# Optimization experiments

Measured on AMD Instinct MI355X. Metric: run time of the kernel, lower is better.

Reference implementation:

```python
import math
import jax, jax.numpy as jnp
import numpy as np

NUM_HEADS = 8


def setup_inputs() -> dict:
    rng = jax.random.key(0)
    ks = jax.random.split(rng, 6)
    S, B, E = 2048, 4, 512
    scale = 1.0 / math.sqrt(E)  # xavier-ish init scale
    return {
        "query": jax.random.normal(ks[0], (S, B, E), jnp.float32),
        "key": jax.random.normal(ks[1], (S, B, E), jnp.float32),
        "value": jax.random.normal(ks[2], (S, B, E), jnp.float32),
        "attn_mask": jax.random.normal(ks[3], (B, S, S), jnp.float32),
        "in_proj_weight": jax.random.normal(ks[4], (3 * E, E), jnp.float32) * scale,
        "in_proj_bias": jnp.zeros((3 * E,), jnp.float32),
        "out_proj_weight": jax.random.normal(ks[5], (E, E), jnp.float32) * scale,
        "out_proj_bias": jnp.zeros((E,), jnp.float32),
    }


def reference(query, key, value, attn_mask, in_proj_weight, in_proj_bias,
              out_proj_weight, out_proj_bias):
    # Layout: [S, B, E] (batch_first=False)
    S, B, E = query.shape
    H = NUM_HEADS
    D = E // H
    w_q, w_k, w_v = jnp.split(in_proj_weight, 3, axis=0)  # each [E, E]
    b_q, b_k, b_v = jnp.split(in_proj_bias, 3)
    q = query @ w_q.T + b_q
    k = key @ w_k.T + b_k
    v = value @ w_v.T + b_v

    def to_heads(x):  # [S,B,E] -> [B,H,S,D]
        return x.reshape(S, B, H, D).transpose(1, 2, 0, 3)

    qh = to_heads(q) * (1.0 / math.sqrt(D))
    kh = to_heads(k)
    vh = to_heads(v)
    # full score matrix [B,H,S,S] with per-batch additive mask broadcast over heads
    scores = jnp.einsum('bhsd,bhtd->bhst', qh, kh) + attn_mask[:, None, :, :]
    attn = jax.nn.softmax(scores, axis=-1)
    out = jnp.einsum('bhst,bhtd->bhsd', attn, vh)
    out = out.transpose(2, 0, 1, 3).reshape(S, B, E)  # back to [S,B,E]
    return out @ out_proj_weight.T + out_proj_bias
```

## Files before the change

kernel.cpp:

```cpp
#include <hip/hip_runtime.h>


#define L2E 1.44269504088896340736f

typedef __attribute__((ext_vector_type(8))) __bf16 bf16x8;
typedef __attribute__((ext_vector_type(4))) float f32x4;
typedef __attribute__((ext_vector_type(16))) float f32x16;

static __device__ __forceinline__ unsigned pk2(float a, float b) {
    union { unsigned u; __bf16 h[2]; } cv;
    cv.h[0] = (__bf16)a; cv.h[1] = (__bf16)b;
    return cv.u;
}

static __device__ __forceinline__ unsigned short f2bf(float f) {
    union { unsigned short s; __bf16 h; } cv;
    cv.h = (__bf16)f;
    return cv.s;
}

static __device__ __forceinline__ float bflo(unsigned u) {
    union { unsigned u; float f; } cv; cv.u = u << 16; return cv.f;
}
static __device__ __forceinline__ float bfhi(unsigned u) {
    union { unsigned u; float f; } cv; cv.u = u & 0xFFFF0000u; return cv.f;
}

__global__ __launch_bounds__(256) void qkv_kernel(
    const float* __restrict__ Xq, const float* __restrict__ Xk,
    const float* __restrict__ Xv, const float* __restrict__ W,
    const float* __restrict__ bias,
    unsigned short* __restrict__ Qp, unsigned short* __restrict__ Kp,
    unsigned short* __restrict__ Vt)
{
    __shared__ unsigned short lA[128][40];
    __shared__ unsigned short lB[128][40];

    const int z = blockIdx.z;
    const float* X  = (z == 0) ? Xq : (z == 1) ? Xk : Xv;
    const float* Wz = W + (size_t)z * 512 * 512;
    const int rb = blockIdx.y * 128;
    const int nb = blockIdx.x * 128;
    const int tid  = threadIdx.x;
    const int lane = tid & 63, wave = tid >> 6;
    const int wr = wave >> 1, wc = wave & 1;
    const int lq = lane & 15, lg = lane >> 4;

    f32x4 acc[4][4];
#pragma unroll
    for (int i = 0; i < 4; ++i)
#pragma unroll
        for (int j = 0; j < 4; ++j) acc[i][j] = (f32x4){0.f, 0.f, 0.f, 0.f};

    const int srow = tid >> 1;
    const int scol = (tid & 1) * 16;

    for (int kt = 0; kt < 16; ++kt) {
        const int k0 = kt * 32;
        if (kt) __syncthreads();
        {
            const float* g = X + (size_t)(rb + srow) * 512 + k0 + scol;
            float4 x0 = *(const float4*)(g + 0);
            float4 x1 = *(const float4*)(g + 4);
            float4 x2 = *(const float4*)(g + 8);
            float4 x3 = *(const float4*)(g + 12);
            uint4 w0, w1;
            w0.x = pk2(x0.x, x0.y); w0.y = pk2(x0.z, x0.w);
            w0.z = pk2(x1.x, x1.y); w0.w = pk2(x1.z, x1.w);
            w1.x = pk2(x2.x, x2.y); w1.y = pk2(x2.z, x2.w);
            w1.z = pk2(x3.x, x3.y); w1.w = pk2(x3.z, x3.w);
            *(uint4*)&lA[srow][scol] = w0;
            *(uint4*)&lA[srow][scol + 8] = w1;
        }
        {
            const float* g = Wz + (size_t)(nb + srow) * 512 + k0 + scol;
            float4 x0 = *(const float4*)(g + 0);
            float4 x1 = *(const float4*)(g + 4);
            float4 x2 = *(const float4*)(g + 8);
            float4 x3 = *(const float4*)(g + 12);
            uint4 w0, w1;
            w0.x = pk2(x0.x, x0.y); w0.y = pk2(x0.z, x0.w);
            w0.z = pk2(x1.x, x1.y); w0.w = pk2(x1.z, x1.w);
            w1.x = pk2(x2.x, x2.y); w1.y = pk2(x2.z, x2.w);
            w1.z = pk2(x3.x, x3.y); w1.w = pk2(x3.z, x3.w);
            *(uint4*)&lB[srow][scol] = w0;
            *(uint4*)&lB[srow][scol + 8] = w1;
        }
        __syncthreads();

        bf16x8 af[4], bf[4];
#pragma unroll
        for (int mi = 0; mi < 4; ++mi)
            af[mi] = *(const bf16x8*)&lA[wr * 64 + mi * 16 + lq][lg * 8];
#pragma unroll
        for (int ni = 0; ni < 4; ++ni)
            bf[ni] = *(const bf16x8*)&lB[wc * 64 + ni * 16 + lq][lg * 8];
#pragma unroll
        for (int mi = 0; mi < 4; ++mi)
#pragma unroll
            for (int ni = 0; ni < 4; ++ni)
                acc[mi][ni] = __builtin_amdgcn_mfma_f32_16x16x32_bf16(
                    af[mi], bf[ni], acc[mi][ni], 0, 0, 0);
    }

    const float* bz = bias + z * 512;
#pragma unroll
    for (int ni = 0; ni < 4; ++ni) {
        const int n = nb + wc * 64 + ni * 16 + lq;
        const float bv = bz[n];
        const int h = n >> 6, d = n & 63;
#pragma unroll
        for (int mi = 0; mi < 4; ++mi) {
#pragma unroll
            for (int r = 0; r < 4; ++r) {
                const int t = rb + wr * 64 + mi * 16 + lg * 4 + r;
                float v = acc[mi][ni][r] + bv;
                const int s = t >> 2, b = t & 3;
                if (z == 0) {
                    v *= 0.125f * L2E;
                    Qp[((size_t)(b * 8 + h) * 2048 + s) * 64 + d] = f2bf(v);
                } else if (z == 1) {
                    Kp[((size_t)(b * 8 + h) * 2048 + s) * 64 + d] = f2bf(v);
                } else {
                    Vt[((size_t)(b * 8 + h) * 64 + d) * 2048 + s] = f2bf(v);
                }
            }
        }
    }
}

__global__ __launch_bounds__(256) void maskprep_kernel(
    const float* __restrict__ mask, unsigned short* __restrict__ Mf)
{
    __shared__ float lT[32][261];
    const int tid = threadIdx.x;
    const int bq = blockIdx.y;
    const int kx = blockIdx.x;
    const float* base = mask + ((size_t)(bq >> 6) * 2048 + (bq & 63) * 32) * 2048
                        + (size_t)kx * 256;

    const int r = tid >> 3, ci = tid & 7;
    const float* rp = base + (size_t)r * 2048;
#pragma unroll
    for (int j = 0; j < 8; ++j) {
        const int c = (ci + j * 8) * 4;
        float4 v = *(const float4*)(rp + c);
        lT[r][c + 0] = v.x * L2E;
        lT[r][c + 1] = v.y * L2E;
        lT[r][c + 2] = v.z * L2E;
        lT[r][c + 3] = v.w * L2E;
    }
    __syncthreads();

    const int w = tid >> 6, lane = tid & 63;
    const int lc = lane & 31, hi = lane >> 5;
#pragma unroll
    for (int t = 0; t < 2; ++t) {
        const int ktl = w * 2 + t;
        float p[16];
#pragma unroll
        for (int jj = 0; jj < 16; ++jj)
            p[jj] = lT[lc][ktl * 32 + (jj & 3) + 8 * (jj >> 2) + 4 * hi];
        unsigned short* dst = Mf + ((size_t)bq * 64 + kx * 8 + ktl) * 1024 + lane * 16;
        *(uint4*)(dst) = make_uint4(pk2(p[0], p[1]), pk2(p[2], p[3]),
                                    pk2(p[4], p[5]), pk2(p[6], p[7]));
        *(uint4*)(dst + 8) = make_uint4(pk2(p[8], p[9]),  pk2(p[10], p[11]),
                                        pk2(p[12], p[13]), pk2(p[14], p[15]));
    }
}

#define SWAP32(a, b) asm("v_permlane32_swap_b32 %0, %1" : "+v"(a), "+v"(b))

#define COMPUTE(KC, VC, M) do {                                                \
    bf16x8 pf[4];                                                              \
    _Pragma("unroll")                                                          \
    for (int kblk = 0; kblk < 2; ++kblk) {                                     \
        f32x16 z;                                                              \
        {                                                                      \
            const uint4 m0 = M[kblk][0], m1 = M[kblk][1];                      \
            z[0]  = bflo(m0.x); z[1]  = bfhi(m0.x);                            \
            z[2]  = bflo(m0.y); z[3]  = bfhi(m0.y);                            \
            z[4]  = bflo(m0.z); z[5]  = bfhi(m0.z);                            \
            z[6]  = bflo(m0.w); z[7]  = bfhi(m0.w);                            \
            z[8]  = bflo(m1.x); z[9]  = bfhi(m1.x);                            \
            z[10] = bflo(m1.y); z[11] = bfhi(m1.y);                            \
            z[12] = bflo(m1.z); z[13] = bfhi(m1.z);                            \
            z[14] = bflo(m1.w); z[15] = bfhi(m1.w);                            \
        }                                                                      \
        __builtin_amdgcn_s_setprio(1);                                         \
        _Pragma("unroll")                                                      \
        for (int s = 0; s < 4; ++s) {                                          \
            bf16x8 kf = *(const bf16x8*)((KC) + fof[kblk][s]);                 \
            z = __builtin_amdgcn_mfma_f32_32x32x16_bf16(kf, qf[s], z, 0,0,0);  \
        }                                                                      \
        __builtin_amdgcn_s_setprio(0);                                         \
        float p[16];                                                           \
        _Pragma("unroll")                                                      \
        for (int i = 0; i < 16; ++i) p[i] = exp2f(z[i]);                       \
        lsum += (((p[0]+p[1])+(p[2]+p[3])) + ((p[4]+p[5])+(p[6]+p[7])))        \
              + (((p[8]+p[9])+(p[10]+p[11])) + ((p[12]+p[13])+(p[14]+p[15]))); \
        unsigned a0 = pk2(p[0], p[1]),   b0 = pk2(p[4], p[5]);                 \
        unsigned a1 = pk2(p[2], p[3]),   b1 = pk2(p[6], p[7]);                 \
        SWAP32(a0, b0); SWAP32(a1, b1);                                        \
        union { unsigned w[4]; bf16x8 v; } u0;                                 \
        u0.w[0] = a0; u0.w[1] = a1; u0.w[2] = b0; u0.w[3] = b1;                \
        pf[kblk*2] = u0.v;                                                     \
        unsigned c0 = pk2(p[8], p[9]),   d0 = pk2(p[12], p[13]);               \
        unsigned c1 = pk2(p[10], p[11]), d1 = pk2(p[14], p[15]);               \
        SWAP32(c0, d0); SWAP32(c1, d1);                                        \
        union { unsigned w[4]; bf16x8 v; } u1;                                 \
        u1.w[0] = c0; u1.w[1] = c1; u1.w[2] = d0; u1.w[3] = d1;                \
        pf[kblk*2+1] = u1.v;                                                   \
    }                                                                          \
    __builtin_amdgcn_s_setprio(1);                                             \
    _Pragma("unroll")                                                          \
    for (int s = 0; s < 4; ++s) {                                              \
        bf16x8 vf0 = *(const bf16x8*)((VC) + fof[0][s]);                       \
        o0 = __builtin_amdgcn_mfma_f32_32x32x16_bf16(vf0, pf[s], o0, 0,0,0);   \
        bf16x8 vf1 = *(const bf16x8*)((VC) + fof[1][s]);                       \
        o1 = __builtin_amdgcn_mfma_f32_32x32x16_bf16(vf1, pf[s], o1, 0,0,0);   \
    }                                                                          \
    __builtin_amdgcn_s_setprio(0);                                             \
} while (0)

#define LOADNEXT(MD) do {                                                      \
    ka = *(const uint4*)(pgK); kc = *(const uint4*)(pgK + 8);                  \
    va = *(const uint4*)(pgV); vc = *(const uint4*)(pgV + 8);                  \
    MD[0][0] = *(const uint4*)(pmf);                                           \
    MD[0][1] = *(const uint4*)(pmf + 8);                                       \
    MD[1][0] = *(const uint4*)(pmf + 1024);                                    \
    MD[1][1] = *(const uint4*)(pmf + 1032);                                    \
    pgK += 4096; pgV += 64; pmf += 2048;                                       \
} while (0)

#define STORE(BUF) do {                                                        \
    *(uint4*)&lK[BUF][srow][su0 * 8] = ka;                                     \
    *(uint4*)&lK[BUF][srow][su1 * 8] = kc;                                     \
    *(uint4*)&lV[BUF][srow][su0 * 8] = va;                                     \
    *(uint4*)&lV[BUF][srow][su1 * 8] = vc;                                     \
} while (0)

__global__ __launch_bounds__(256, 2) void attn_kernel(
    const unsigned short* __restrict__ Qp, const unsigned short* __restrict__ Kp,
    const unsigned short* __restrict__ Vt, const unsigned short* __restrict__ Mf,
    unsigned short* __restrict__ AO)
{
    __shared__ unsigned short lK[2][64][64];
    __shared__ unsigned short lV[2][64][64];

    const int bh = blockIdx.y;
    const int b = bh >> 3, h = bh & 7;
    const int qb = blockIdx.x * 128;
    const int tid  = threadIdx.x;
    const int lane = tid & 63, wave = tid >> 6;
    const int lc = lane & 31, hi = lane >> 5;
    const int qg = qb + wave * 32 + lc;

    bf16x8 qf[4];
    {
        const unsigned short* qp = Qp + ((size_t)bh * 2048 + qg) * 64 + hi * 8;
#pragma unroll
        for (int s = 0; s < 4; ++s)
            qf[s] = *(const bf16x8*)(qp + s * 16);
    }

    f32x16 o0, o1;
#pragma unroll
    for (int i = 0; i < 16; ++i) { o0[i] = 0.f; o1[i] = 0.f; }
    float lsum = 0.f;

    int fof[2][4];
#pragma unroll
    for (int blk = 0; blk < 2; ++blk)
#pragma unroll
        for (int s = 0; s < 4; ++s)
            fof[blk][s] = (blk * 32 + lc) * 128 +
                          ((((s << 1) | hi) ^ (lane & 7)) * 16);

    const char* lK0c = (const char*)&lK[0][0][0];
    const char* lK1c = (const char*)&lK[1][0][0];
    const char* lV0c = (const char*)&lV[0][0][0];
    const char* lV1c = (const char*)&lV[1][0][0];

    const int srow = tid >> 2;
    const int scu  = (tid & 3) * 2;
    const int su0  = (scu    ) ^ (srow & 7);
    const int su1  = (scu + 1) ^ (srow & 7);
    const unsigned short* pgK = Kp + (size_t)bh * 2048 * 64 + (size_t)srow * 64 + scu * 8;
    const unsigned short* pgV = Vt + (size_t)bh * 64 * 2048 + (size_t)srow * 2048 + scu * 8;
    const unsigned short* pmf = Mf +
        ((size_t)(b * 64 + (qb >> 5) + wave) * 64) * 1024 + lane * 16;

    uint4 ka, kc, va, vc;
    uint4 mA[2][2], mB[2][2];

    LOADNEXT(mA);
    STORE(0);
    __syncthreads();

    for (int kb2 = 0; kb2 < 16; ++kb2) {
        {
            LOADNEXT(mB);
            COMPUTE(lK0c, lV0c, mA);
            STORE(1);
            __syncthreads();
        }
        {
            if (kb2 < 15) LOADNEXT(mA);
            COMPUTE(lK1c, lV1c, mB);
            if (kb2 < 15) {
                STORE(0);
                __syncthreads();
            }
        }
    }

    lsum += __shfl_xor(lsum, 32);
    const float inv = 1.0f / lsum;

    unsigned short* ao = AO + ((size_t)qg * 4 + b) * 512 + h * 64;
#pragma unroll
    for (int g = 0; g < 4; ++g) {
        const int d0 = g * 8 + hi * 4;
        *(uint2*)(ao + d0) =
            make_uint2(pk2(o0[4*g+0] * inv, o0[4*g+1] * inv),
                       pk2(o0[4*g+2] * inv, o0[4*g+3] * inv));
        *(uint2*)(ao + 32 + d0) =
            make_uint2(pk2(o1[4*g+0] * inv, o1[4*g+1] * inv),
                       pk2(o1[4*g+2] * inv, o1[4*g+3] * inv));
    }
}

__global__ __launch_bounds__(256) void oproj_kernel(
    const unsigned short* __restrict__ A, const float* __restrict__ W,
    const float* __restrict__ bias, float* __restrict__ out)
{
    __shared__ unsigned short lA[128][40];
    __shared__ unsigned short lB[128][40];

    const int rb = blockIdx.y * 128;
    const int nb = blockIdx.x * 128;
    const int tid  = threadIdx.x;
    const int lane = tid & 63, wave = tid >> 6;
    const int wr = wave >> 1, wc = wave & 1;
    const int lq = lane & 15, lg = lane >> 4;

    f32x4 acc[4][4];
#pragma unroll
    for (int i = 0; i < 4; ++i)
#pragma unroll
        for (int j = 0; j < 4; ++j) acc[i][j] = (f32x4){0.f, 0.f, 0.f, 0.f};

    const int srow = tid >> 1;
    const int scol = (tid & 1) * 16;

    for (int kt = 0; kt < 16; ++kt) {
        const int k0 = kt * 32;
        if (kt) __syncthreads();
        {
            const unsigned short* g = A + (size_t)(rb + srow) * 512 + k0 + scol;
            *(uint4*)&lA[srow][scol]     = *(const uint4*)g;
            *(uint4*)&lA[srow][scol + 8] = *(const uint4*)(g + 8);
        }
        {
            const float* g = W + (size_t)(nb + srow) * 512 + k0 + scol;
            float4 x0 = *(const float4*)(g + 0);
            float4 x1 = *(const float4*)(g + 4);
            float4 x2 = *(const float4*)(g + 8);
            float4 x3 = *(const float4*)(g + 12);
            uint4 w0, w1;
            w0.x = pk2(x0.x, x0.y); w0.y = pk2(x0.z, x0.w);
            w0.z = pk2(x1.x, x1.y); w0.w = pk2(x1.z, x1.w);
            w1.x = pk2(x2.x, x2.y); w1.y = pk2(x2.z, x2.w);
            w1.z = pk2(x3.x, x3.y); w1.w = pk2(x3.z, x3.w);
            *(uint4*)&lB[srow][scol] = w0;
            *(uint4*)&lB[srow][scol + 8] = w1;
        }
        __syncthreads();

        bf16x8 af[4], bfr[4];
#pragma unroll
        for (int mi = 0; mi < 4; ++mi)
            af[mi] = *(const bf16x8*)&lA[wr * 64 + mi * 16 + lq][lg * 8];
#pragma unroll
        for (int ni = 0; ni < 4; ++ni)
            bfr[ni] = *(const bf16x8*)&lB[wc * 64 + ni * 16 + lq][lg * 8];
#pragma unroll
        for (int mi = 0; mi < 4; ++mi)
#pragma unroll
            for (int ni = 0; ni < 4; ++ni)
                acc[mi][ni] = __builtin_amdgcn_mfma_f32_16x16x32_bf16(
                    af[mi], bfr[ni], acc[mi][ni], 0, 0, 0);
    }

#pragma unroll
    for (int ni = 0; ni < 4; ++ni) {
        const int n = nb + wc * 64 + ni * 16 + lq;
        const float bv = bias[n];
#pragma unroll
        for (int mi = 0; mi < 4; ++mi) {
#pragma unroll
            for (int r = 0; r < 4; ++r) {
                const int t = rb + wr * 64 + mi * 16 + lg * 4 + r;
                out[(size_t)t * 512 + n] = acc[mi][ni][r] + bv;
            }
        }
    }
}

extern "C" void kernel_launch(void* const* d_in, const int* in_sizes, int n_in,
                              void* d_out, int out_size, void* d_ws, size_t ws_size,
                              hipStream_t stream)
{
    (void)in_sizes; (void)n_in; (void)out_size; (void)ws_size;
    const float* query = (const float*)d_in[0];
    const float* key   = (const float*)d_in[1];
    const float* value = (const float*)d_in[2];
    const float* mask  = (const float*)d_in[3];
    const float* w_in  = (const float*)d_in[4];
    const float* b_in  = (const float*)d_in[5];
    const float* w_out = (const float*)d_in[6];
    const float* b_out = (const float*)d_in[7];
    float* out = (float*)d_out;

    char* ws = (char*)d_ws;
    unsigned short* Qp = (unsigned short*)(ws);
    unsigned short* Kp = (unsigned short*)(ws + (size_t)8 * 1024 * 1024);
    unsigned short* Vt = (unsigned short*)(ws + (size_t)16 * 1024 * 1024);
    unsigned short* AO = (unsigned short*)(ws + (size_t)24 * 1024 * 1024);
    unsigned short* Mf = (unsigned short*)(ws + (size_t)32 * 1024 * 1024);

    qkv_kernel<<<dim3(4, 64, 3), 256, 0, stream>>>(query, key, value, w_in, b_in,
                                                   Qp, Kp, Vt);
    maskprep_kernel<<<dim3(8, 256), 256, 0, stream>>>(mask, Mf);
    attn_kernel<<<dim3(16, 32), 256, 0, stream>>>(Qp, Kp, Vt, Mf, AO);
    oproj_kernel<<<dim3(4, 64), 256, 0, stream>>>(AO, w_out, b_out, out);
}
```

Measured before the change: 154.2 us.

## Split attention key range across two wave groups with LDS reduction

Doubles the attention block to 512 threads. Two wave groups each process half of the key sequence for the same 128 queries, using separate double-buffered K/V LDS tiles. Partial outputs and row sums are then combined through shared memory before normalisation and store. This gives 512 blocks of 8 waves instead of 4, raising parallelism and latency hiding. The cost is 64KB of LDS per block, an extra reduction and barrier, and reliance on the softmax having no running max, so partials can simply be added.

```diff
diff --git a/kernel.cpp b/kernel.cpp
--- a/kernel.cpp
+++ b/kernel.cpp
@@ -234,27 +234,30 @@
 } while (0)
 
 #define STORE(BUF) do {                                                        \
-    *(uint4*)&lK[BUF][srow][su0 * 8] = ka;                                     \
-    *(uint4*)&lK[BUF][srow][su1 * 8] = kc;                                     \
-    *(uint4*)&lV[BUF][srow][su0 * 8] = va;                                     \
-    *(uint4*)&lV[BUF][srow][su1 * 8] = vc;                                     \
+    *(uint4*)&lK[kg][BUF][srow][su0 * 8] = ka;                                 \
+    *(uint4*)&lK[kg][BUF][srow][su1 * 8] = kc;                                 \
+    *(uint4*)&lV[kg][BUF][srow][su0 * 8] = va;                                 \
+    *(uint4*)&lV[kg][BUF][srow][su1 * 8] = vc;                                 \
 } while (0)
 
-__global__ __launch_bounds__(256, 2) void attn_kernel(
+__global__ __launch_bounds__(512, 4) void attn_kernel(
     const unsigned short* __restrict__ Qp, const unsigned short* __restrict__ Kp,
     const unsigned short* __restrict__ Vt, const unsigned short* __restrict__ Mf,
     unsigned short* __restrict__ AO)
 {
-    __shared__ unsigned short lK[2][64][64];
-    __shared__ unsigned short lV[2][64][64];
+    __shared__ __align__(16) char smem[65536];
+    unsigned short (*lK)[2][64][64] = (unsigned short (*)[2][64][64])(smem);
+    unsigned short (*lV)[2][64][64] = (unsigned short (*)[2][64][64])(smem + 32768);
+    float* ex = (float*)smem;
 
     const int bh = blockIdx.y;
     const int b = bh >> 3, h = bh & 7;
     const int qb = blockIdx.x * 128;
     const int tid  = threadIdx.x;
     const int lane = tid & 63, wave = tid >> 6;
+    const int qw = wave & 3, kg = wave >> 2;
     const int lc = lane & 31, hi = lane >> 5;
-    const int qg = qb + wave * 32 + lc;
+    const int qg = qb + qw * 32 + lc;
 
     bf16x8 qf[4];
     {
@@ -277,19 +280,22 @@
             fof[blk][s] = (blk * 32 + lc) * 128 +
                           ((((s << 1) | hi) ^ (lane & 7)) * 16);
 
-    const char* lK0c = (const char*)&lK[0][0][0];
-    const char* lK1c = (const char*)&lK[1][0][0];
-    const char* lV0c = (const char*)&lV[0][0][0];
-    const char* lV1c = (const char*)&lV[1][0][0];
-
-    const int srow = tid >> 2;
-    const int scu  = (tid & 3) * 2;
+    const char* lK0c = (const char*)&lK[kg][0][0][0];
+    const char* lK1c = (const char*)&lK[kg][1][0][0];
+    const char* lV0c = (const char*)&lV[kg][0][0][0];
+    const char* lV1c = (const char*)&lV[kg][1][0][0];
+
+    const int gtid = tid & 255;
+    const int srow = gtid >> 2;
+    const int scu  = (gtid & 3) * 2;
     const int su0  = (scu    ) ^ (srow & 7);
     const int su1  = (scu + 1) ^ (srow & 7);
-    const unsigned short* pgK = Kp + (size_t)bh * 2048 * 64 + (size_t)srow * 64 + scu * 8;
-    const unsigned short* pgV = Vt + (size_t)bh * 64 * 2048 + (size_t)srow * 2048 + scu * 8;
+    const unsigned short* pgK = Kp + (size_t)bh * 2048 * 64
+                                + (size_t)(kg * 1024 + srow) * 64 + scu * 8;
+    const unsigned short* pgV = Vt + (size_t)bh * 64 * 2048
+                                + (size_t)srow * 2048 + kg * 1024 + scu * 8;
     const unsigned short* pmf = Mf +
-        ((size_t)(b * 64 + (qb >> 5) + wave) * 64) * 1024 + lane * 16;
+        ((size_t)(b * 64 + (qb >> 5) + qw) * 64 + kg * 32) * 1024 + lane * 16;
 
     uint4 ka, kc, va, vc;
     uint4 mA[2][2], mB[2][2];
@@ -298,7 +304,7 @@
     STORE(0);
     __syncthreads();
 
-    for (int kb2 = 0; kb2 < 16; ++kb2) {
+    for (int kb2 = 0; kb2 < 8; ++kb2) {
         {
             LOADNEXT(mB);
             COMPUTE(lK0c, lV0c, mA);
@@ -306,28 +312,58 @@
             __syncthreads();
         }
         {
-            if (kb2 < 15) LOADNEXT(mA);
+            if (kb2 < 7) LOADNEXT(mA);
             COMPUTE(lK1c, lV1c, mB);
-            if (kb2 < 15) {
+            if (kb2 < 7) {
                 STORE(0);
                 __syncthreads();
             }
         }
     }
+    __syncthreads();
 
     lsum += __shfl_xor(lsum, 32);
-    const float inv = 1.0f / lsum;
+
+    {
+        float* slot = ex + ((size_t)wave * 64 + lane) * 18;
+        if (kg == 0) {
+#pragma unroll
+            for (int i = 0; i < 8; ++i)
+                *(float2*)(slot + 2 * i) = make_float2(o1[2*i], o1[2*i+1]);
+        } else {
+#pragma unroll
+            for (int i = 0; i < 8; ++i)
+                *(float2*)(slot + 2 * i) = make_float2(o0[2*i], o0[2*i+1]);
+        }
+        slot[16] = lsum;
+    }
+    __syncthreads();
+
+    const float* pslot = ex + ((size_t)(wave ^ 4) * 64 + lane) * 18;
+    const float lt = lsum + pslot[16];
+    const float inv = 1.0f / lt;
 
     unsigned short* ao = AO + ((size_t)qg * 4 + b) * 512 + h * 64;
-#pragma unroll
-    for (int g = 0; g < 4; ++g) {
-        const int d0 = g * 8 + hi * 4;
-        *(uint2*)(ao + d0) =
-            make_uint2(pk2(o0[4*g+0] * inv, o0[4*g+1] * inv),
-                       pk2(o0[4*g+2] * inv, o0[4*g+3] * inv));
-        *(uint2*)(ao + 32 + d0) =
-            make_uint2(pk2(o1[4*g+0] * inv, o1[4*g+1] * inv),
-                       pk2(o1[4*g+2] * inv, o1[4*g+3] * inv));
+    if (kg == 0) {
+#pragma unroll
+        for (int g = 0; g < 4; ++g) {
+            const int d0 = g * 8 + hi * 4;
+            float s0 = (o0[4*g+0] + pslot[4*g+0]) * inv;
+            float s1 = (o0[4*g+1] + pslot[4*g+1]) * inv;
+            float s2 = (o0[4*g+2] + pslot[4*g+2]) * inv;
+            float s3 = (o0[4*g+3] + pslot[4*g+3]) * inv;
+            *(uint2*)(ao + d0) = make_uint2(pk2(s0, s1), pk2(s2, s3));
+        }
+    } else {
+#pragma unroll
+        for (int g = 0; g < 4; ++g) {
+            const int d0 = g * 8 + hi * 4;
+            float s0 = (o1[4*g+0] + pslot[4*g+0]) * inv;
+            float s1 = (o1[4*g+1] + pslot[4*g+1]) * inv;
+            float s2 = (o1[4*g+2] + pslot[4*g+2]) * inv;
+            float s3 = (o1[4*g+3] + pslot[4*g+3]) * inv;
+            *(uint2*)(ao + 32 + d0) = make_uint2(pk2(s0, s1), pk2(s2, s3));
+        }
     }
 }
 
@@ -433,6 +469,6 @@
     qkv_kernel<<<dim3(4, 64, 3), 256, 0, stream>>>(query, key, value, w_in, b_in,
                                                    Qp, Kp, Vt);
     maskprep_kernel<<<dim3(8, 256), 256, 0, stream>>>(mask, Mf);
-    attn_kernel<<<dim3(16, 32), 256, 0, stream>>>(Qp, Kp, Vt, Mf, AO);
+    attn_kernel<<<dim3(16, 32), 512, 0, stream>>>(Qp, Kp, Vt, Mf, AO);
     oproj_kernel<<<dim3(4, 64), 256, 0, stream>>>(AO, w_out, b_out, out);
 }
```

New measurement: 268.7 us. 74.2% more time.

## Split attention over key halves and merge QKV projection with mask prep

Applied to the files above, without the earlier changes.

The attention kernel is split into two key-range halves (grid z=2). Each half writes unnormalized fp32 partial outputs and row sums, and a new reduce kernel adds the halves, normalizes and converts to bf16. This doubles the attention grid from 512 to 1024 blocks for better CU occupancy. The QKV projection and mask-prep kernels are also fused into one launch with a block-index switch, removing one launch and letting the two workloads overlap. The cost is extra fp32 partial traffic (about 32MB written and read) and an added reduce launch. The merge is correct without a max rescale only if the softmax is computed without per-row max subtraction, which is not visible here.

```diff
diff --git a/kernel.cpp b/kernel.cpp
--- a/kernel.cpp
+++ b/kernel.cpp
@@ -26,146 +26,147 @@
     union { unsigned u; float f; } cv; cv.u = u & 0xFFFF0000u; return cv.f;
 }
 
-__global__ __launch_bounds__(256) void qkv_kernel(
+__global__ __launch_bounds__(256) void qkvmask_kernel(
     const float* __restrict__ Xq, const float* __restrict__ Xk,
     const float* __restrict__ Xv, const float* __restrict__ W,
-    const float* __restrict__ bias,
+    const float* __restrict__ bias, const float* __restrict__ mask,
     unsigned short* __restrict__ Qp, unsigned short* __restrict__ Kp,
-    unsigned short* __restrict__ Vt)
+    unsigned short* __restrict__ Vt, unsigned short* __restrict__ Mf)
 {
-    __shared__ unsigned short lA[128][40];
-    __shared__ unsigned short lB[128][40];
-
-    const int z = blockIdx.z;
-    const float* X  = (z == 0) ? Xq : (z == 1) ? Xk : Xv;
-    const float* Wz = W + (size_t)z * 512 * 512;
-    const int rb = blockIdx.y * 128;
-    const int nb = blockIdx.x * 128;
-    const int tid  = threadIdx.x;
-    const int lane = tid & 63, wave = tid >> 6;
-    const int wr = wave >> 1, wc = wave & 1;
-    const int lq = lane & 15, lg = lane >> 4;
-
-    f32x4 acc[4][4];
-#pragma unroll
-    for (int i = 0; i < 4; ++i)
-#pragma unroll
-        for (int j = 0; j < 4; ++j) acc[i][j] = (f32x4){0.f, 0.f, 0.f, 0.f};
-
-    const int srow = tid >> 1;
-    const int scol = (tid & 1) * 16;
-
-    for (int kt = 0; kt < 16; ++kt) {
-        const int k0 = kt * 32;
-        if (kt) __syncthreads();
-        {
-            const float* g = X + (size_t)(rb + srow) * 512 + k0 + scol;
-            float4 x0 = *(const float4*)(g + 0);
-            float4 x1 = *(const float4*)(g + 4);
-            float4 x2 = *(const float4*)(g + 8);
-            float4 x3 = *(const float4*)(g + 12);
-            uint4 w0, w1;
-            w0.x = pk2(x0.x, x0.y); w0.y = pk2(x0.z, x0.w);
-            w0.z = pk2(x1.x, x1.y); w0.w = pk2(x1.z, x1.w);
-            w1.x = pk2(x2.x, x2.y); w1.y = pk2(x2.z, x2.w);
-            w1.z = pk2(x3.x, x3.y); w1.w = pk2(x3.z, x3.w);
-            *(uint4*)&lA[srow][scol] = w0;
-            *(uint4*)&lA[srow][scol + 8] = w1;
-        }
-        {
-            const float* g = Wz + (size_t)(nb + srow) * 512 + k0 + scol;
-            float4 x0 = *(const float4*)(g + 0);
-            float4 x1 = *(const float4*)(g + 4);
-            float4 x2 = *(const float4*)(g + 8);
-            float4 x3 = *(const float4*)(g + 12);
-            uint4 w0, w1;
-            w0.x = pk2(x0.x, x0.y); w0.y = pk2(x0.z, x0.w);
-            w0.z = pk2(x1.x, x1.y); w0.w = pk2(x1.z, x1.w);
-            w1.x = pk2(x2.x, x2.y); w1.y = pk2(x2.z, x2.w);
-            w1.z = pk2(x3.x, x3.y); w1.w = pk2(x3.z, x3.w);
-            *(uint4*)&lB[srow][scol] = w0;
-            *(uint4*)&lB[srow][scol + 8] = w1;
-        }
-        __syncthreads();
-
-        bf16x8 af[4], bf[4];
-#pragma unroll
-        for (int mi = 0; mi < 4; ++mi)
-            af[mi] = *(const bf16x8*)&lA[wr * 64 + mi * 16 + lq][lg * 8];
-#pragma unroll
-        for (int ni = 0; ni < 4; ++ni)
-            bf[ni] = *(const bf16x8*)&lB[wc * 64 + ni * 16 + lq][lg * 8];
-#pragma unroll
-        for (int mi = 0; mi < 4; ++mi)
+    __shared__ __align__(16) char smem[33408];
+    const int id = blockIdx.x;
+    const int tid = threadIdx.x;
+
+    if (id < 768) {
+        unsigned short (*lA)[40] = (unsigned short (*)[40])smem;
+        unsigned short (*lB)[40] = (unsigned short (*)[40])(smem + 10240);
+
+        const int z = id >> 8;
+        const float* X  = (z == 0) ? Xq : (z == 1) ? Xk : Xv;
+        const float* Wz = W + (size_t)z * 512 * 512;
+        const int rb = ((id >> 2) & 63) * 128;
+        const int nb = (id & 3) * 128;
+        const int lane = tid & 63, wave = tid >> 6;
+        const int wr = wave >> 1, wc = wave & 1;
+        const int lq = lane & 15, lg = lane >> 4;
+
+        f32x4 acc[4][4];
+#pragma unroll
+        for (int i = 0; i < 4; ++i)
+#pragma unroll
+            for (int j = 0; j < 4; ++j) acc[i][j] = (f32x4){0.f, 0.f, 0.f, 0.f};
+
+        const int srow = tid >> 1;
+        const int scol = (tid & 1) * 16;
+
+        for (int kt = 0; kt < 16; ++kt) {
+            const int k0 = kt * 32;
+            if (kt) __syncthreads();
+            {
+                const float* g = X + (size_t)(rb + srow) * 512 + k0 + scol;
+                float4 x0 = *(const float4*)(g + 0);
+                float4 x1 = *(const float4*)(g + 4);
+                float4 x2 = *(const float4*)(g + 8);
+                float4 x3 = *(const float4*)(g + 12);
+                uint4 w0, w1;
+                w0.x = pk2(x0.x, x0.y); w0.y = pk2(x0.z, x0.w);
+                w0.z = pk2(x1.x, x1.y); w0.w = pk2(x1.z, x1.w);
+                w1.x = pk2(x2.x, x2.y); w1.y = pk2(x2.z, x2.w);
+                w1.z = pk2(x3.x, x3.y); w1.w = pk2(x3.z, x3.w);
+                *(uint4*)&lA[srow][scol] = w0;
+                *(uint4*)&lA[srow][scol + 8] = w1;
+            }
+            {
+                const float* g = Wz + (size_t)(nb + srow) * 512 + k0 + scol;
+                float4 x0 = *(const float4*)(g + 0);
+                float4 x1 = *(const float4*)(g + 4);
+                float4 x2 = *(const float4*)(g + 8);
+                float4 x3 = *(const float4*)(g + 12);
+                uint4 w0, w1;
+                w0.x = pk2(x0.x, x0.y); w0.y = pk2(x0.z, x0.w);
+                w0.z = pk2(x1.x, x1.y); w0.w = pk2(x1.z, x1.w);
+                w1.x = pk2(x2.x, x2.y); w1.y = pk2(x2.z, x2.w);
+                w1.z = pk2(x3.x, x3.y); w1.w = pk2(x3.z, x3.w);
+                *(uint4*)&lB[srow][scol] = w0;
+                *(uint4*)&lB[srow][scol + 8] = w1;
+            }
+            __syncthreads();
+
+            bf16x8 af[4], bf[4];
+#pragma unroll
+            for (int mi = 0; mi < 4; ++mi)
+                af[mi] = *(const bf16x8*)&lA[wr * 64 + mi * 16 + lq][lg * 8];
 #pragma unroll
             for (int ni = 0; ni < 4; ++ni)
-                acc[mi][ni] = __builtin_amdgcn_mfma_f32_16x16x32_bf16(
-                    af[mi], bf[ni], acc[mi][ni], 0, 0, 0);
-    }
-
-    const float* bz = bias + z * 512;
-#pragma unroll
-    for (int ni = 0; ni < 4; ++ni) {
-        const int n = nb + wc * 64 + ni * 16 + lq;
-        const float bv = bz[n];
-        const int h = n >> 6, d = n & 63;
-#pragma unroll
-        for (int mi = 0; mi < 4; ++mi) {
-#pragma unroll
-            for (int r = 0; r < 4; ++r) {
-                const int t = rb + wr * 64 + mi * 16 + lg * 4 + r;
-                float v = acc[mi][ni][r] + bv;
-                const int s = t >> 2, b = t & 3;
-                if (z == 0) {
-                    v *= 0.125f * L2E;
-                    Qp[((size_t)(b * 8 + h) * 2048 + s) * 64 + d] = f2bf(v);
-                } else if (z == 1) {
-                    Kp[((size_t)(b * 8 + h) * 2048 + s) * 64 + d] = f2bf(v);
-                } else {
-                    Vt[((size_t)(b * 8 + h) * 64 + d) * 2048 + s] = f2bf(v);
+                bf[ni] = *(const bf16x8*)&lB[wc * 64 + ni * 16 + lq][lg * 8];
+#pragma unroll
+            for (int mi = 0; mi < 4; ++mi)
+#pragma unroll
+                for (int ni = 0; ni < 4; ++ni)
+                    acc[mi][ni] = __builtin_amdgcn_mfma_f32_16x16x32_bf16(
+                        af[mi], bf[ni], acc[mi][ni], 0, 0, 0);
+        }
+
+        const float* bz = bias + z * 512;
+#pragma unroll
+        for (int ni = 0; ni < 4; ++ni) {
+            const int n = nb + wc * 64 + ni * 16 + lq;
+            const float bv = bz[n];
+            const int h = n >> 6, d = n & 63;
+#pragma unroll
+            for (int mi = 0; mi < 4; ++mi) {
+#pragma unroll
+                for (int r = 0; r < 4; ++r) {
+                    const int t = rb + wr * 64 + mi * 16 + lg * 4 + r;
+                    float v = acc[mi][ni][r] + bv;
+                    const int s = t >> 2, b = t & 3;
+                    if (z == 0) {
+                        v *= 0.125f * L2E;
+                        Qp[((size_t)(b * 8 + h) * 2048 + s) * 64 + d] = f2bf(v);
+                    } else if (z == 1) {
+                        Kp[((size_t)(b * 8 + h) * 2048 + s) * 64 + d] = f2bf(v);
+                    } else {
+                        Vt[((size_t)(b * 8 + h) * 64 + d) * 2048 + s] = f2bf(v);
+                    }
                 }
             }
         }
-    }
-}
-
-__global__ __launch_bounds__(256) void maskprep_kernel(
-    const float* __restrict__ mask, unsigned short* __restrict__ Mf)
-{
-    __shared__ float lT[32][261];
-    const int tid = threadIdx.x;
-    const int bq = blockIdx.y;
-    const int kx = blockIdx.x;
-    const float* base = mask + ((size_t)(bq >> 6) * 2048 + (bq & 63) * 32) * 2048
-                        + (size_t)kx * 256;
-
-    const int r = tid >> 3, ci = tid & 7;
-    const float* rp = base + (size_t)r * 2048;
-#pragma unroll
-    for (int j = 0; j < 8; ++j) {
-        const int c = (ci + j * 8) * 4;
-        float4 v = *(const float4*)(rp + c);
-        lT[r][c + 0] = v.x * L2E;
-        lT[r][c + 1] = v.y * L2E;
-        lT[r][c + 2] = v.z * L2E;
-        lT[r][c + 3] = v.w * L2E;
-    }
-    __syncthreads();
-
-    const int w = tid >> 6, lane = tid & 63;
-    const int lc = lane & 31, hi = lane >> 5;
-#pragma unroll
-    for (int t = 0; t < 2; ++t) {
-        const int ktl = w * 2 + t;
-        float p[16];
-#pragma unroll
-        for (int jj = 0; jj < 16; ++jj)
-            p[jj] = lT[lc][ktl * 32 + (jj & 3) + 8 * (jj >> 2) + 4 * hi];
-        unsigned short* dst = Mf + ((size_t)bq * 64 + kx * 8 + ktl) * 1024 + lane * 16;
-        *(uint4*)(dst) = make_uint4(pk2(p[0], p[1]), pk2(p[2], p[3]),
-                                    pk2(p[4], p[5]), pk2(p[6], p[7]));
-        *(uint4*)(dst + 8) = make_uint4(pk2(p[8], p[9]),  pk2(p[10], p[11]),
-                                        pk2(p[12], p[13]), pk2(p[14], p[15]));
+    } else {
+        float (*lT)[261] = (float (*)[261])smem;
+        const int m = id - 768;
+        const int kx = m & 7;
+        const int bq = m >> 3;
+        const float* base = mask + ((size_t)(bq >> 6) * 2048 + (bq & 63) * 32) * 2048
+                            + (size_t)kx * 256;
+
+        const int r = tid >> 3, ci = tid & 7;
+        const float* rp = base + (size_t)r * 2048;
+#pragma unroll
+        for (int j = 0; j < 8; ++j) {
+            const int c = (ci + j * 8) * 4;
+            float4 v = *(const float4*)(rp + c);
+            lT[r][c + 0] = v.x * L2E;
+            lT[r][c + 1] = v.y * L2E;
+            lT[r][c + 2] = v.z * L2E;
+            lT[r][c + 3] = v.w * L2E;
+        }
+        __syncthreads();
+
+        const int w = tid >> 6, lane = tid & 63;
+        const int lc = lane & 31, hi = lane >> 5;
+#pragma unroll
+        for (int t = 0; t < 2; ++t) {
+            const int ktl = w * 2 + t;
+            float p[16];
+#pragma unroll
+            for (int jj = 0; jj < 16; ++jj)
+                p[jj] = lT[lc][ktl * 32 + (jj & 3) + 8 * (jj >> 2) + 4 * hi];
+            unsigned short* dst = Mf + ((size_t)bq * 64 + kx * 8 + ktl) * 1024 + lane * 16;
+            *(uint4*)(dst) = make_uint4(pk2(p[0], p[1]), pk2(p[2], p[3]),
+                                        pk2(p[4], p[5]), pk2(p[6], p[7]));
+            *(uint4*)(dst + 8) = make_uint4(pk2(p[8], p[9]),  pk2(p[10], p[11]),
+                                            pk2(p[12], p[13]), pk2(p[14], p[15]));
+        }
     }
 }
 
@@ -243,7 +244,7 @@
 __global__ __launch_bounds__(256, 2) void attn_kernel(
     const unsigned short* __restrict__ Qp, const unsigned short* __restrict__ Kp,
     const unsigned short* __restrict__ Vt, const unsigned short* __restrict__ Mf,
-    unsigned short* __restrict__ AO)
+    float* __restrict__ Op, float* __restrict__ Ls)
 {
     __shared__ unsigned short lK[2][64][64];
     __shared__ unsigned short lV[2][64][64];
@@ -251,6 +252,7 @@
     const int bh = blockIdx.y;
     const int b = bh >> 3, h = bh & 7;
     const int qb = blockIdx.x * 128;
+    const int kg = blockIdx.z;
     const int tid  = threadIdx.x;
     const int lane = tid & 63, wave = tid >> 6;
     const int lc = lane & 31, hi = lane >> 5;
@@ -286,10 +288,12 @@
     const int scu  = (tid & 3) * 2;
     const int su0  = (scu    ) ^ (srow & 7);
     const int su1  = (scu + 1) ^ (srow & 7);
-    const unsigned short* pgK = Kp + (size_t)bh * 2048 * 64 + (size_t)srow * 64 + scu * 8;
-    const unsigned short* pgV = Vt + (size_t)bh * 64 * 2048 + (size_t)srow * 2048 + scu * 8;
+    const unsigned short* pgK = Kp + (size_t)bh * 2048 * 64
+                                + (size_t)(kg * 1024 + srow) * 64 + scu * 8;
+    const unsigned short* pgV = Vt + (size_t)bh * 64 * 2048
+                                + (size_t)srow * 2048 + kg * 1024 + scu * 8;
     const unsigned short* pmf = Mf +
-        ((size_t)(b * 64 + (qb >> 5) + wave) * 64) * 1024 + lane * 16;
+        ((size_t)(b * 64 + (qb >> 5) + wave) * 64 + kg * 32) * 1024 + lane * 16;
 
     uint4 ka, kc, va, vc;
     uint4 mA[2][2], mB[2][2];
@@ -298,7 +302,7 @@
     STORE(0);
     __syncthreads();
 
-    for (int kb2 = 0; kb2 < 16; ++kb2) {
+    for (int kb2 = 0; kb2 < 8; ++kb2) {
         {
             LOADNEXT(mB);
             COMPUTE(lK0c, lV0c, mA);
@@ -306,9 +310,9 @@
             __syncthreads();
         }
         {
-            if (kb2 < 15) LOADNEXT(mA);
+            if (kb2 < 7) LOADNEXT(mA);
             COMPUTE(lK1c, lV1c, mB);
-            if (kb2 < 15) {
+            if (kb2 < 7) {
                 STORE(0);
                 __syncthreads();
             }
@@ -316,19 +320,32 @@
     }
 
     lsum += __shfl_xor(lsum, 32);
-    const float inv = 1.0f / lsum;
-
-    unsigned short* ao = AO + ((size_t)qg * 4 + b) * 512 + h * 64;
+
+    float* op = Op + (size_t)kg * 4194304 + ((size_t)qg * 4 + b) * 512 + h * 64;
 #pragma unroll
     for (int g = 0; g < 4; ++g) {
         const int d0 = g * 8 + hi * 4;
-        *(uint2*)(ao + d0) =
-            make_uint2(pk2(o0[4*g+0] * inv, o0[4*g+1] * inv),
-                       pk2(o0[4*g+2] * inv, o0[4*g+3] * inv));
-        *(uint2*)(ao + 32 + d0) =
-            make_uint2(pk2(o1[4*g+0] * inv, o1[4*g+1] * inv),
-                       pk2(o1[4*g+2] * inv, o1[4*g+3] * inv));
-    }
+        *(float4*)(op + d0)      = make_float4(o0[4*g+0], o0[4*g+1], o0[4*g+2], o0[4*g+3]);
+        *(float4*)(op + 32 + d0) = make_float4(o1[4*g+0], o1[4*g+1], o1[4*g+2], o1[4*g+3]);
+    }
+    if (lane < 32)
+        Ls[(size_t)kg * 65536 + (size_t)bh * 2048 + qg] = lsum;
+}
+
+__global__ __launch_bounds__(256) void reduce_kernel(
+    const float* __restrict__ Op, const float* __restrict__ Ls,
+    unsigned short* __restrict__ AO)
+{
+    const int i4 = blockIdx.x * 256 + threadIdx.x;
+    const int i = i4 * 4;
+    const int qg = i >> 11;
+    const int bh = (((i >> 9) & 3) << 3) | ((i >> 6) & 7);
+    const float l = Ls[(size_t)bh * 2048 + qg] + Ls[65536 + (size_t)bh * 2048 + qg];
+    const float inv = 1.0f / l;
+    float4 a = *(const float4*)(Op + i);
+    float4 c = *(const float4*)(Op + 4194304 + i);
+    *(uint2*)(AO + i) = make_uint2(pk2((a.x + c.x) * inv, (a.y + c.y) * inv),
+                                   pk2((a.z + c.z) * inv, (a.w + c.w) * inv));
 }
 
 __global__ __launch_bounds__(256) void oproj_kernel(
@@ -424,15 +441,18 @@
     float* out = (float*)d_out;
 
     char* ws = (char*)d_ws;
+    const size_t MB = 1024 * 1024;
     unsigned short* Qp = (unsigned short*)(ws);
-    unsigned short* Kp = (unsigned short*)(ws + (size_t)8 * 1024 * 1024);
-    unsigned short* Vt = (unsigned short*)(ws + (size_t)16 * 1024 * 1024);
-    unsigned short* AO = (unsigned short*)(ws + (size_t)24 * 1024 * 1024);
-    unsigned short* Mf = (unsigned short*)(ws + (size_t)32 * 1024 * 1024);
-
-    qkv_kernel<<<dim3(4, 64, 3), 256, 0, stream>>>(query, key, value, w_in, b_in,
-                                                   Qp, Kp, Vt);
-    maskprep_kernel<<<dim3(8, 256), 256, 0, stream>>>(mask, Mf);
-    attn_kernel<<<dim3(16, 32), 256, 0, stream>>>(Qp, Kp, Vt, Mf, AO);
+    unsigned short* Kp = (unsigned short*)(ws + 8 * MB);
+    unsigned short* Vt = (unsigned short*)(ws + 16 * MB);
+    unsigned short* AO = (unsigned short*)(ws + 24 * MB);
+    unsigned short* Mf = (unsigned short*)(ws + 32 * MB);
+    float*          Op = (float*)(ws + 64 * MB);
+    float*          Ls = (float*)(ws + 96 * MB);
+
+    qkvmask_kernel<<<dim3(2816), 256, 0, stream>>>(query, key, value, w_in, b_in,
+                                                   mask, Qp, Kp, Vt, Mf);
+    attn_kernel<<<dim3(16, 32, 2), 256, 0, stream>>>(Qp, Kp, Vt, Mf, Op, Ls);
+    reduce_kernel<<<dim3(4096), 256, 0, stream>>>(Op, Ls, AO);
     oproj_kernel<<<dim3(4, 64), 256, 0, stream>>>(AO, w_out, b_out, out);
 }
```

Result: no change. 153.2 us (-0.6%).
